# Kernel tuning notes

Measured on AMD Instinct MI355X. Metric: run time of the kernel, lower is better.

The kernel has to match this reference:

```python
import jax, jax.numpy as jnp
from jax import lax
import numpy as np

T, B, I, H, OUT = 1024, 32, 128, 512, 10


def _lstm_layer(x, W_ih, W_hh, b):
    """PyTorch-convention LSTM layer. x: [T,B,in], W_ih: [4H,in], W_hh: [4H,H], b: [4H].
    Gate order: i, f, g, o. Returns all hidden states [T,B,H]."""
    hdim = W_hh.shape[1]
    # Precompute input projections for all timesteps (big GEMM, compute-bound).
    x_proj = jnp.einsum('tbi,gi->tbg', x, W_ih) + b  # [T,B,4H]

    def step(carry, xp_t):
        h, c = carry
        gates = xp_t + h @ W_hh.T  # [B,4H]
        i_g, f_g, g_g, o_g = jnp.split(gates, 4, axis=-1)
        i_g = jax.nn.sigmoid(i_g)
        f_g = jax.nn.sigmoid(f_g)
        g_g = jnp.tanh(g_g)
        o_g = jax.nn.sigmoid(o_g)
        c = f_g * c + i_g * g_g
        h = o_g * jnp.tanh(c)
        return (h, c), h

    h0 = jnp.zeros((x.shape[1], hdim), x.dtype)
    c0 = jnp.zeros((x.shape[1], hdim), x.dtype)
    _, hs = lax.scan(step, (h0, c0), x_proj)
    return hs  # [T,B,H]


def setup_inputs() -> dict:
    key = jax.random.key(0)
    ks = jax.random.split(key, 9)
    s1 = 1.0 / np.sqrt(H)  # PyTorch LSTM init scale U(-1/sqrt(H), 1/sqrt(H)); use scaled normal
    return {
        'data': jax.random.normal(ks[0], (T, B, I), jnp.float32),
        'W_ih1': jax.random.normal(ks[1], (4 * H, I), jnp.float32) * s1,
        'W_hh1': jax.random.normal(ks[2], (4 * H, H), jnp.float32) * s1,
        'b1': jax.random.normal(ks[3], (4 * H,), jnp.float32) * s1,
        'W_ih2': jax.random.normal(ks[4], (4 * H, H), jnp.float32) * s1,
        'W_hh2': jax.random.normal(ks[5], (4 * H, H), jnp.float32) * s1,
        'b2': jax.random.normal(ks[6], (4 * H,), jnp.float32) * s1,
        'W3': jax.random.normal(ks[7], (OUT, H), jnp.float32) * s1,
        'b3': jax.random.normal(ks[8], (OUT,), jnp.float32) * s1,
    }


def reference(data, W_ih1, W_hh1, b1, W_ih2, W_hh2, b2, W3, b3):
    h = _lstm_layer(data, W_ih1, W_hh1, b1)   # [T,B,H]
    h = _lstm_layer(h, W_ih2, W_hh2, b2)      # [T,B,H]
    logits = jnp.einsum('tbh,oh->tbo', h, W3) + b3  # [T,B,OUT]
    return jax.nn.softmax(logits, axis=2)
```

## Files before the change

kernel.cpp:

```cpp
#include <hip/hip_runtime.h>
#include <cstdint>
#include <cstddef>

#define TCHUNK 128
#define NCHUNK 8
#define BATCH 32
#define IDIM 128
#define HDIM 512
#define GDIM 2048
#define ODIM 10
#define NBLK 256
#define XPSTEP (GDIM * BATCH)
#define SLAB_F 16384
#define SLAB_B (SLAB_F * 4)

typedef float f4 __attribute__((ext_vector_type(4)));
typedef float f2 __attribute__((ext_vector_type(2)));

__device__ __forceinline__ void llc_store(float* p, float v) {
  asm volatile("global_store_dword %0, %1, off sc0 sc1" :: "v"(p), "v"(v) : "memory");
}
__device__ __forceinline__ float quad_sum(float x) {
  int t = __builtin_amdgcn_update_dpp(0, __float_as_int(x), 0xB1, 0xF, 0xF, true);
  x += __int_as_float(t);
  t = __builtin_amdgcn_update_dpp(0, __float_as_int(x), 0x4E, 0xF, 0xF, true);
  x += __int_as_float(t);
  return x;
}

#define BARRIER() do {                                                      \
    asm volatile("s_waitcnt lgkmcnt(0)" ::: "memory");                      \
    __builtin_amdgcn_sched_barrier(0);                                      \
    __builtin_amdgcn_s_barrier();                                           \
    __builtin_amdgcn_sched_barrier(0);                                      \
  } while (0)

template<int K>
__launch_bounds__(256, 2)
__global__ void proj_kernel(const float* __restrict__ X,
                            const float* __restrict__ W,
                            const float* __restrict__ bias,
                            float* __restrict__ P) {
  __shared__ float Xs[8][132];
  __shared__ float Ws[8][132];
  const int tid = threadIdx.x;
  const int n0 = blockIdx.x * 128;
  const int m0 = blockIdx.y * 128;
  const int tx = tid & 15, ty = tid >> 4;
  const int lm = tid >> 1;
  const int kq = (tid & 1) * 4;
  f2 acc2[8][4];
#pragma unroll
  for (int i = 0; i < 8; ++i)
#pragma unroll
    for (int j = 0; j < 4; ++j) acc2[i][j] = (f2){0.f, 0.f};

  for (int k0 = 0; k0 < K; k0 += 8) {
    const float4 xv = *(const float4*)&X[(size_t)(m0 + lm) * K + k0 + kq];
    const float4 wv = *(const float4*)&W[(size_t)(n0 + lm) * K + k0 + kq];
    __syncthreads();
    Xs[kq + 0][lm] = xv.x; Xs[kq + 1][lm] = xv.y; Xs[kq + 2][lm] = xv.z; Xs[kq + 3][lm] = xv.w;
    Ws[kq + 0][lm] = wv.x; Ws[kq + 1][lm] = wv.y; Ws[kq + 2][lm] = wv.z; Ws[kq + 3][lm] = wv.w;
    __syncthreads();
#pragma unroll
    for (int kk = 0; kk < 8; ++kk) {
      float a[8];
      *(float4*)&a[0] = *(const float4*)&Xs[kk][ty * 8];
      *(float4*)&a[4] = *(const float4*)&Xs[kk][ty * 8 + 4];
      f2 b2[4];
#pragma unroll
      for (int jp = 0; jp < 4; ++jp) b2[jp] = *(const f2*)&Ws[kk][tx * 8 + 2 * jp];
#pragma unroll
      for (int i = 0; i < 8; ++i)
#pragma unroll
        for (int jp = 0; jp < 4; ++jp) acc2[i][jp] += b2[jp] * a[i];
    }
  }
  const int mb = m0 + ty * 8;
  const int t  = mb >> 5;
  const int b0 = mb & 31;
#pragma unroll
  for (int j = 0; j < 8; ++j) {
    const int n = n0 + tx * 8 + j;
    const float bj = bias[n];
    float* dst = &P[((size_t)t * GDIM + n) * BATCH + b0];
#pragma unroll
    for (int i = 0; i < 8; ++i)
      dst[i] = ((j & 1) ? acc2[i][j >> 1].y : acc2[i][j >> 1].x) + bj;
  }
}

__launch_bounds__(256, 1)
__global__ void scan_kernel(const float* __restrict__ xp,
                            const float* __restrict__ Whh,
                            float* __restrict__ hout,
                            float* __restrict__ hb,
                            float* __restrict__ ccur,
                            int first) {
  __shared__ float h_s[2112];
  __shared__ float red[1024];
  __shared__ float gate_s[256];
  __shared__ float pad[17408];

  const int tid = threadIdx.x, bid = blockIdx.x;
  const int g = bid & 7, rank = bid >> 3, slot16 = rank * 16;
  const int w = tid >> 6, l = tid & 63;
  const int s4 = l & 3, rq = l >> 2;
  const int sg = 4 * w + s4;
  const int cx = sg & 7;
  const int kb = 32 * sg;

  float wreg[4][32];
#pragma unroll
  for (int r = 0; r < 4; ++r) {
    const int rl = 4 * rq + r;
    const float* wp = Whh + (size_t)((rl >> 4) * HDIM + slot16 + (rl & 15)) * HDIM + kb;
#pragma unroll
    for (int e = 0; e < 32; ++e) wreg[r][e] = wp[e ^ cx];
  }

  const int cl = l >> 4, m = l & 15;
  const int sgS = 4 * w + (m >> 2);
  const int sig = sgS & 7;
  int dsaddr[8];
#pragma unroll
  for (int i = 0; i < 8; ++i)
    dsaddr[i] = 132 * sgS + 4 * (8 * (m & 3) + (i ^ sig)) + cl;
  const int srcoff = cl * 512 + 128 * w + 8 * m;

  const int qg = tid >> 6, jg = (tid >> 2) & 15, bg = tid & 3;
  const float* xq = xp + (size_t)(qg * HDIM + slot16 + jg) * BATCH + g * 4 + bg;

  const int jj = l >> 2, bb = l & 3;

  float c_st = 0.f;
  if (!first && w == 0) c_st = ccur[(size_t)(g * 4 + bb) * HDIM + slot16 + jj];

  const float* hptr = &h_s[132 * sg];

#pragma unroll 1
  for (int tt = 0; tt < TCHUNK; ++tt) {
    const float* src = hb + (size_t)tt * SLAB_F + g * 2048 + srcoff;
    f4 va, vb;
    int guard = 0;
    while (true) {
      asm volatile("global_load_dwordx4 %0, %2, off sc0 sc1\n\t"
                   "global_load_dwordx4 %1, %3, off sc0 sc1\n\t"
                   "s_waitcnt vmcnt(0)"
                   : "=&v"(va), "=&v"(vb) : "v"(src), "v"(src + 4) : "memory");
      const bool ok =
          __float_as_uint(va.x) != 0xFFFFFFFFu && __float_as_uint(va.y) != 0xFFFFFFFFu &&
          __float_as_uint(va.z) != 0xFFFFFFFFu && __float_as_uint(va.w) != 0xFFFFFFFFu &&
          __float_as_uint(vb.x) != 0xFFFFFFFFu && __float_as_uint(vb.y) != 0xFFFFFFFFu &&
          __float_as_uint(vb.z) != 0xFFFFFFFFu && __float_as_uint(vb.w) != 0xFFFFFFFFu;
      if (__all(ok) || ++guard > 100000) break;
      __builtin_amdgcn_s_sleep(1);
    }
    h_s[dsaddr[0]] = va.x; h_s[dsaddr[1]] = va.y;
    h_s[dsaddr[2]] = va.z; h_s[dsaddr[3]] = va.w;
    h_s[dsaddr[4]] = vb.x; h_s[dsaddr[5]] = vb.y;
    h_s[dsaddr[6]] = vb.z; h_s[dsaddr[7]] = vb.w;
    const float xpv = xq[(size_t)tt * XPSTEP];
    BARRIER();

    f2 a01[4], a23[4];
#pragma unroll
    for (int r = 0; r < 4; ++r) { a01[r] = (f2){0.f, 0.f}; a23[r] = (f2){0.f, 0.f}; }
#pragma unroll
    for (int kk = 0; kk < 32; ++kk) {
      const f4 hv = *(const f4*)&hptr[4 * kk];
      const f2 h01 = {hv.x, hv.y}, h23 = {hv.z, hv.w};
#pragma unroll
      for (int r = 0; r < 4; ++r) {
        a01[r] += h01 * wreg[r][kk];
        a23[r] += h23 * wreg[r][kk];
      }
    }
#pragma unroll
    for (int r = 0; r < 4; ++r) {
      a01[r].x = quad_sum(a01[r].x); a01[r].y = quad_sum(a01[r].y);
      a23[r].x = quad_sum(a23[r].x); a23[r].y = quad_sum(a23[r].y);
    }
    f2 r01, r23;
    { const f2 v0 = (s4 & 1) ? a01[1] : a01[0];
      const f2 v1 = (s4 & 1) ? a01[3] : a01[2];
      r01 = (s4 & 2) ? v1 : v0;
      const f2 u0 = (s4 & 1) ? a23[1] : a23[0];
      const f2 u1 = (s4 & 1) ? a23[3] : a23[2];
      r23 = (s4 & 2) ? u1 : u0; }
    *(f4*)&red[(w << 8) + 4 * l] = (f4){r01.x, r01.y, r23.x, r23.y};
    BARRIER();

    const float pre = red[tid] + red[256 + tid] + red[512 + tid] + red[768 + tid] + xpv;
    gate_s[tid] = (qg == 2) ? tanhf(pre) : 1.f / (1.f + __expf(-pre));
    BARRIER();

    if (w == 0) {
      const float ig = gate_s[jj * 4 + bb];
      const float fg = gate_s[64 + jj * 4 + bb];
      const float gg = gate_s[128 + jj * 4 + bb];
      const float og = gate_s[192 + jj * 4 + bb];
      c_st = fg * c_st + ig * gg;
      const float hval = og * tanhf(c_st);
      llc_store(hb + (size_t)(tt + 1) * SLAB_F + g * 2048 + bb * 512 + slot16 + jj, hval);
      hout[(size_t)tt * (BATCH * HDIM) + (size_t)(g * 4 + bb) * HDIM + slot16 + jj] = hval;
    }
  }
  if (w == 0) ccur[(size_t)(g * 4 + bb) * HDIM + slot16 + jj] = c_st;
  ((volatile float*)pad)[tid] = c_st;
}

__launch_bounds__(256, 2)
__global__ void head_kernel(const float* __restrict__ h2,
                            const float* __restrict__ W3,
                            const float* __restrict__ b3,
                            float* __restrict__ outp) {
  const int tid = threadIdx.x;
  const int lane = tid & 63;
  const int wv = tid >> 6;
  const int row = blockIdx.x * 4 + wv;
  const float* hrow = &h2[(size_t)row * HDIM];
  float hreg[8];
  *(float4*)&hreg[0] = *(const float4*)&hrow[lane * 8];
  *(float4*)&hreg[4] = *(const float4*)&hrow[lane * 8 + 4];
  float logit[ODIM];
#pragma unroll
  for (int o = 0; o < ODIM; ++o) {
    const float* wrow = &W3[o * HDIM + lane * 8];
    float w[8];
    *(float4*)&w[0] = *(const float4*)&wrow[0];
    *(float4*)&w[4] = *(const float4*)&wrow[4];
    float pp = 0.f;
#pragma unroll
    for (int j = 0; j < 8; ++j) pp += hreg[j] * w[j];
#pragma unroll
    for (int off = 32; off > 0; off >>= 1) pp += __shfl_xor(pp, off);
    logit[o] = pp + b3[o];
  }
  float mx = logit[0];
#pragma unroll
  for (int o = 1; o < ODIM; ++o) mx = fmaxf(mx, logit[o]);
  float ssum = 0.f;
#pragma unroll
  for (int o = 0; o < ODIM; ++o) { logit[o] = __expf(logit[o] - mx); ssum += logit[o]; }
  const float inv = 1.f / ssum;
  if (lane == 0) {
    float* dst = &outp[(size_t)row * ODIM];
#pragma unroll
    for (int o = 0; o < ODIM; ++o) dst[o] = logit[o] * inv;
  }
}

extern "C" void kernel_launch(void* const* d_in, const int* in_sizes, int n_in,
                              void* d_out, int out_size, void* d_ws, size_t ws_size,
                              hipStream_t stream) {
  const float* data  = (const float*)d_in[0];
  const float* W_ih1 = (const float*)d_in[1];
  const float* W_hh1 = (const float*)d_in[2];
  const float* b1    = (const float*)d_in[3];
  const float* W_ih2 = (const float*)d_in[4];
  const float* W_hh2 = (const float*)d_in[5];
  const float* b2    = (const float*)d_in[6];
  const float* W3    = (const float*)d_in[7];
  const float* b3    = (const float*)d_in[8];
  float* outp = (float*)d_out;

  char* ws = (char*)d_ws;
  size_t off = 0;
  float* xp    = (float*)(ws + off); off += (size_t)TCHUNK * GDIM * BATCH * 4;
  float* h1c   = (float*)(ws + off); off += (size_t)TCHUNK * BATCH * HDIM * 4;
  float* h2c   = (float*)(ws + off); off += (size_t)TCHUNK * BATCH * HDIM * 4;
  float* hb1   = (float*)(ws + off); off += (size_t)(TCHUNK + 1) * SLAB_B;
  float* hb2   = (float*)(ws + off); off += (size_t)(TCHUNK + 1) * SLAB_B;
  float* ccur1 = (float*)(ws + off); off += BATCH * HDIM * 4;
  float* ccur2 = (float*)(ws + off); off += BATCH * HDIM * 4;
  if (off > ws_size) return;

  hipMemsetAsync(hb1, 0x00, SLAB_B, stream);
  hipMemsetAsync((char*)hb1 + SLAB_B, 0xFF, (size_t)TCHUNK * SLAB_B, stream);
  hipMemsetAsync(hb2, 0x00, SLAB_B, stream);
  hipMemsetAsync((char*)hb2 + SLAB_B, 0xFF, (size_t)TCHUNK * SLAB_B, stream);

  const dim3 pgrid(GDIM / 128, (TCHUNK * BATCH) / 128);
  for (int c = 0; c < NCHUNK; ++c) {
    const float* xin = data + (size_t)c * TCHUNK * BATCH * IDIM;
    proj_kernel<IDIM><<<pgrid, 256, 0, stream>>>(xin, W_ih1, b1, xp);
    scan_kernel<<<NBLK, 256, 0, stream>>>(xp, W_hh1, h1c, hb1, ccur1, c == 0);
    if (c < NCHUNK - 1) {
      hipMemcpyAsync(hb1, (char*)hb1 + (size_t)TCHUNK * SLAB_B, SLAB_B,
                     hipMemcpyDeviceToDevice, stream);
      hipMemsetAsync((char*)hb1 + SLAB_B, 0xFF, (size_t)TCHUNK * SLAB_B, stream);
    }
    proj_kernel<HDIM><<<pgrid, 256, 0, stream>>>(h1c, W_ih2, b2, xp);
    scan_kernel<<<NBLK, 256, 0, stream>>>(xp, W_hh2, h2c, hb2, ccur2, c == 0);
    if (c < NCHUNK - 1) {
      hipMemcpyAsync(hb2, (char*)hb2 + (size_t)TCHUNK * SLAB_B, SLAB_B,
                     hipMemcpyDeviceToDevice, stream);
      hipMemsetAsync((char*)hb2 + SLAB_B, 0xFF, (size_t)TCHUNK * SLAB_B, stream);
    }
    head_kernel<<<(TCHUNK * BATCH) / 4, 256, 0, stream>>>(
        h2c, W3, b3, outp + (size_t)c * TCHUNK * BATCH * ODIM);
  }
}
```

Baseline: 8.744 ms.

## Duplicate hidden-state exchange into L2-local and LLC buffers, poll both

Result: slower. 9.676 ms (+10.7%).

```diff
diff --git a/kernel.cpp b/kernel.cpp
--- a/kernel.cpp
+++ b/kernel.cpp
@@ -34,6 +34,11 @@
     __builtin_amdgcn_s_barrier();                                           \
     __builtin_amdgcn_sched_barrier(0);                                      \
   } while (0)
+
+#define OK8(A, B) (__float_as_uint(A.x) != 0xFFFFFFFFu && __float_as_uint(A.y) != 0xFFFFFFFFu && \
+                   __float_as_uint(A.z) != 0xFFFFFFFFu && __float_as_uint(A.w) != 0xFFFFFFFFu && \
+                   __float_as_uint(B.x) != 0xFFFFFFFFu && __float_as_uint(B.y) != 0xFFFFFFFFu && \
+                   __float_as_uint(B.z) != 0xFFFFFFFFu && __float_as_uint(B.w) != 0xFFFFFFFFu)
 
 template<int K>
 __launch_bounds__(256, 2)
@@ -94,7 +99,8 @@
 __global__ void scan_kernel(const float* __restrict__ xp,
                             const float* __restrict__ Whh,
                             float* __restrict__ hout,
-                            float* __restrict__ hb,
+                            float* __restrict__ hb2,
+                            float* __restrict__ hbL,
                             float* __restrict__ ccur,
                             int first) {
   __shared__ float h_s[2112];
@@ -140,20 +146,26 @@
 
 #pragma unroll 1
   for (int tt = 0; tt < TCHUNK; ++tt) {
-    const float* src = hb + (size_t)tt * SLAB_F + g * 2048 + srcoff;
+    const float* s2 = hb2 + (size_t)tt * SLAB_F + g * 2048 + srcoff;
+    const float* sL = hbL + (size_t)tt * SLAB_F + g * 2048 + srcoff;
     f4 va, vb;
     int guard = 0;
     while (true) {
-      asm volatile("global_load_dwordx4 %0, %2, off sc0 sc1\n\t"
-                   "global_load_dwordx4 %1, %3, off sc0 sc1\n\t"
+      f4 a2, b2v, aL, bL;
+      asm volatile("global_load_dwordx4 %0, %4, off sc0\n\t"
+                   "global_load_dwordx4 %1, %4, off offset:16 sc0\n\t"
+                   "global_load_dwordx4 %2, %5, off sc0 sc1\n\t"
+                   "global_load_dwordx4 %3, %5, off offset:16 sc0 sc1\n\t"
                    "s_waitcnt vmcnt(0)"
-                   : "=&v"(va), "=&v"(vb) : "v"(src), "v"(src + 4) : "memory");
-      const bool ok =
-          __float_as_uint(va.x) != 0xFFFFFFFFu && __float_as_uint(va.y) != 0xFFFFFFFFu &&
-          __float_as_uint(va.z) != 0xFFFFFFFFu && __float_as_uint(va.w) != 0xFFFFFFFFu &&
-          __float_as_uint(vb.x) != 0xFFFFFFFFu && __float_as_uint(vb.y) != 0xFFFFFFFFu &&
-          __float_as_uint(vb.z) != 0xFFFFFFFFu && __float_as_uint(vb.w) != 0xFFFFFFFFu;
-      if (__all(ok) || ++guard > 100000) break;
+                   : "=&v"(a2), "=&v"(b2v), "=&v"(aL), "=&v"(bL)
+                   : "v"(s2), "v"(sL) : "memory");
+      const bool ok2 = OK8(a2, b2v);
+      const bool okL = OK8(aL, bL);
+      if (__all(ok2 | okL) || ++guard > 200000) {
+        va = ok2 ? a2 : aL;
+        vb = ok2 ? b2v : bL;
+        break;
+      }
       __builtin_amdgcn_s_sleep(1);
     }
     h_s[dsaddr[0]] = va.x; h_s[dsaddr[1]] = va.y;
@@ -202,7 +214,9 @@
       const float og = gate_s[192 + jj * 4 + bb];
       c_st = fg * c_st + ig * gg;
       const float hval = og * tanhf(c_st);
-      llc_store(hb + (size_t)(tt + 1) * SLAB_F + g * 2048 + bb * 512 + slot16 + jj, hval);
+      const size_t ho = (size_t)(tt + 1) * SLAB_F + g * 2048 + bb * 512 + slot16 + jj;
+      hb2[ho] = hval;
+      llc_store(hbL + ho, hval);
       hout[(size_t)tt * (BATCH * HDIM) + (size_t)(g * 4 + bb) * HDIM + slot16 + jj] = hval;
     }
   }
@@ -270,35 +284,41 @@
   float* xp    = (float*)(ws + off); off += (size_t)TCHUNK * GDIM * BATCH * 4;
   float* h1c   = (float*)(ws + off); off += (size_t)TCHUNK * BATCH * HDIM * 4;
   float* h2c   = (float*)(ws + off); off += (size_t)TCHUNK * BATCH * HDIM * 4;
-  float* hb1   = (float*)(ws + off); off += (size_t)(TCHUNK + 1) * SLAB_B;
-  float* hb2   = (float*)(ws + off); off += (size_t)(TCHUNK + 1) * SLAB_B;
+  float* hb2a  = (float*)(ws + off); off += (size_t)(TCHUNK + 1) * SLAB_B;
+  float* hbLa  = (float*)(ws + off); off += (size_t)(TCHUNK + 1) * SLAB_B;
+  float* hb2b  = (float*)(ws + off); off += (size_t)(TCHUNK + 1) * SLAB_B;
+  float* hbLb  = (float*)(ws + off); off += (size_t)(TCHUNK + 1) * SLAB_B;
   float* ccur1 = (float*)(ws + off); off += BATCH * HDIM * 4;
   float* ccur2 = (float*)(ws + off); off += BATCH * HDIM * 4;
   if (off > ws_size) return;
 
-  hipMemsetAsync(hb1, 0x00, SLAB_B, stream);
-  hipMemsetAsync((char*)hb1 + SLAB_B, 0xFF, (size_t)TCHUNK * SLAB_B, stream);
-  hipMemsetAsync(hb2, 0x00, SLAB_B, stream);
-  hipMemsetAsync((char*)hb2 + SLAB_B, 0xFF, (size_t)TCHUNK * SLAB_B, stream);
+  hipMemsetAsync(hb2a, 0x00, SLAB_B, stream);
+  hipMemsetAsync((char*)hb2a + SLAB_B, 0xFF, (size_t)TCHUNK * SLAB_B, stream);
+  hipMemsetAsync(hbLa, 0x00, SLAB_B, stream);
+  hipMemsetAsync((char*)hbLa + SLAB_B, 0xFF, (size_t)TCHUNK * SLAB_B, stream);
+  hipMemsetAsync(hb2b, 0x00, SLAB_B, stream);
+  hipMemsetAsync((char*)hb2b + SLAB_B, 0xFF, (size_t)TCHUNK * SLAB_B, stream);
+  hipMemsetAsync(hbLb, 0x00, SLAB_B, stream);
+  hipMemsetAsync((char*)hbLb + SLAB_B, 0xFF, (size_t)TCHUNK * SLAB_B, stream);
 
   const dim3 pgrid(GDIM / 128, (TCHUNK * BATCH) / 128);
+
+#define RECYCLE(HB) do {                                                    \
+    hipMemcpyAsync(HB, (char*)HB + (size_t)TCHUNK * SLAB_B, SLAB_B,         \
+                   hipMemcpyDeviceToDevice, stream);                        \
+    hipMemsetAsync((char*)HB + SLAB_B, 0xFF, (size_t)TCHUNK * SLAB_B, stream); \
+  } while (0)
+
   for (int c = 0; c < NCHUNK; ++c) {
     const float* xin = data + (size_t)c * TCHUNK * BATCH * IDIM;
     proj_kernel<IDIM><<<pgrid, 256, 0, stream>>>(xin, W_ih1, b1, xp);
-    scan_kernel<<<NBLK, 256, 0, stream>>>(xp, W_hh1, h1c, hb1, ccur1, c == 0);
-    if (c < NCHUNK - 1) {
-      hipMemcpyAsync(hb1, (char*)hb1 + (size_t)TCHUNK * SLAB_B, SLAB_B,
-                     hipMemcpyDeviceToDevice, stream);
-      hipMemsetAsync((char*)hb1 + SLAB_B, 0xFF, (size_t)TCHUNK * SLAB_B, stream);
-    }
+    scan_kernel<<<NBLK, 256, 0, stream>>>(xp, W_hh1, h1c, hb2a, hbLa, ccur1, c == 0);
+    if (c < NCHUNK - 1) { RECYCLE(hb2a); RECYCLE(hbLa); }
     proj_kernel<HDIM><<<pgrid, 256, 0, stream>>>(h1c, W_ih2, b2, xp);
-    scan_kernel<<<NBLK, 256, 0, stream>>>(xp, W_hh2, h2c, hb2, ccur2, c == 0);
-    if (c < NCHUNK - 1) {
-      hipMemcpyAsync(hb2, (char*)hb2 + (size_t)TCHUNK * SLAB_B, SLAB_B,
-                     hipMemcpyDeviceToDevice, stream);
-      hipMemsetAsync((char*)hb2 + SLAB_B, 0xFF, (size_t)TCHUNK * SLAB_B, stream);
-    }
+    scan_kernel<<<NBLK, 256, 0, stream>>>(xp, W_hh2, h2c, hb2b, hbLb, ccur2, c == 0);
+    if (c < NCHUNK - 1) { RECYCLE(hb2b); RECYCLE(hbLb); }
     head_kernel<<<(TCHUNK * BATCH) / 4, 256, 0, stream>>>(
         h2c, W3, b3, outp + (size_t)c * TCHUNK * BATCH * ODIM);
   }
-}
+#undef RECYCLE
+}
```
